# Kernel tuning notes

Measured on AMD Instinct MI355X. Metric: run time of the kernel, lower is better.

Reference implementation:

```python
import math
import jax, jax.numpy as jnp
import numpy as np

B, L, D, H, DK = 2, 2048, 1024, 16, 64
LATTICE = (4, 4)


def _build_neighbours(n_heads, shape):
    positions = [divmod(i, shape[1]) for i in range(n_heads)]
    idx = np.full((n_heads, 8), -1, dtype=np.int32)
    w = np.zeros((n_heads, 8), dtype=np.float32)
    for i, (r1, c1) in enumerate(positions):
        k = 0
        for dr in (-1, 0, 1):
            for dc in (-1, 0, 1):
                if dr == 0 and dc == 0:
                    continue
                if k >= 8:
                    break
                tgt = (r1 + dr, c1 + dc)
                for j, p in enumerate(positions):
                    if p == tgt:
                        idx[i, k] = j
                        w[i, k] = math.exp(-math.hypot(dr, dc))
                        k += 1
                        break
    return idx, w


def setup_inputs() -> dict:
    key = jax.random.key(0)
    ks = jax.random.split(key, 8)
    s = 1.0 / math.sqrt(D)  # typical linear init scale
    nb_idx, nb_w = _build_neighbours(H, LATTICE)
    return {
        "query": jax.random.normal(ks[0], (B, L, D), jnp.float32),
        "key": jax.random.normal(ks[1], (B, L, D), jnp.float32),
        "value": jax.random.normal(ks[2], (B, L, D), jnp.float32),
        "Wq": jax.random.normal(ks[3], (H, DK, D), jnp.float32) * s,
        "Wk": jax.random.normal(ks[4], (H, DK, D), jnp.float32) * s,
        "Wv": jax.random.normal(ks[5], (H, DK, D), jnp.float32) * s,
        "coupling_strength": jnp.full((H,), 0.1, jnp.float32),
        "out_w": jax.random.normal(ks[6], (D, D), jnp.float32) * s,
        "out_b": jnp.zeros((D,), jnp.float32),
        "neighbour_w": jnp.asarray(nb_w),
        "mask": jax.random.randint(ks[7], (B, L), 0, 2, jnp.int32),
        "neighbour_idx": jnp.asarray(nb_idx),
    }


def _phases(coupling_strength, neighbour_idx, neighbour_w):
    # Sequential Kuramoto update over heads (order matters: earlier heads'
    # updated phases are visible to later heads, as in the torch loop).
    freq = 1.0 + 0.1 * jnp.arange(H, dtype=jnp.float32)
    ph = jnp.zeros((H,), jnp.float32)
    two_pi = 2.0 * math.pi
    for i in range(H):  # H=16, structurally distinct sequential states
        nb = jnp.clip(neighbour_idx[i], 0, H - 1)  # invalid slots have w==0
        coupling = jnp.sum(neighbour_w[i] * jnp.sin(ph[nb] - ph[i]))
        new = jnp.mod(ph[i] + 0.01 * (freq[i] + coupling_strength[i] * coupling), two_pi)
        ph = ph.at[i].set(new)
    return ph


def reference(query, key, value, Wq, Wk, Wv, coupling_strength, out_w, out_b,
              neighbour_w, mask, neighbour_idx):
    ph = _phases(coupling_strength, neighbour_idx, neighbour_w)
    bias = 0.1 * jnp.cos(ph)  # [H] per-head scalar bias

    # Batched per-head projections: [B,L,D] x [H,DK,D] -> [B,H,L,DK]
    Q = jnp.einsum('bld,hkd->bhlk', query, Wq)
    K = jnp.einsum('bld,hkd->bhlk', key, Wk)
    V = jnp.einsum('bld,hkd->bhlk', value, Wv)

    scale = math.sqrt(float(DK))
    scores = jnp.einsum('bhqd,bhkd->bhqk', Q, K) / scale  # [B,H,L,L]
    scores = scores + bias[None, :, None, None]
    m = mask[:, None, None, :]  # [B,1,1,L], matches mask.unsqueeze(1).unsqueeze(1)
    scores = jnp.where(m == 0, jnp.float32(-10000.0), scores)
    attn = jax.nn.softmax(scores, axis=-1)
    out = jnp.einsum('bhqk,bhkd->bhqd', attn, V)  # [B,H,L,DK]
    out = out.transpose(0, 2, 1, 3).reshape(B, L, H * DK)  # concat heads
    return out @ out_w.T + out_b
```

## Files before the change

### kernel.cpp

```cpp
#include <hip/hip_runtime.h>
#include <hip/hip_fp16.h>


#define B_ 2
#define L_ 2048
#define D_ 1024
#define H_ 16
#define DK_ 64

#define QSCALE 0.1803368801111244f
#define MASKOFF -14427.0f

typedef _Float16 f16;
typedef _Float16 f16x2 __attribute__((ext_vector_type(2)));
typedef _Float16 f16x4 __attribute__((ext_vector_type(4)));
typedef _Float16 f16x8 __attribute__((ext_vector_type(8)));
typedef __fp16 hf16x2 __attribute__((ext_vector_type(2)));
typedef float f32x4 __attribute__((ext_vector_type(4)));

static __device__ __forceinline__ float fast_exp2(float x) {
    float r;
    asm("v_exp_f32 %0, %1" : "=v"(r) : "v"(x));
    return r;
}

static __device__ __forceinline__ f16x4 pack4(float a, float b, float c, float d) {
    hf16x2 lo = __builtin_amdgcn_cvt_pkrtz(a, b);
    hf16x2 hi = __builtin_amdgcn_cvt_pkrtz(c, d);
    f16x2 l2 = __builtin_bit_cast(f16x2, lo);
    f16x2 h2 = __builtin_bit_cast(f16x2, hi);
    f16x4 o; o[0] = l2[0]; o[1] = l2[1]; o[2] = h2[0]; o[3] = h2[1];
    return o;
}

__global__ __launch_bounds__(256) void qkv_proj_kernel(
    const float* __restrict__ query, const float* __restrict__ keyx,
    const float* __restrict__ value,
    const float* __restrict__ Wq, const float* __restrict__ Wk,
    const float* __restrict__ Wv,
    f16* __restrict__ Qh, f16* __restrict__ Kh, f16* __restrict__ VhT)
{
    const int z = blockIdx.z;
    const float* X = (z == 0) ? query : (z == 1) ? keyx : value;
    const float* W = (z == 0) ? Wq : (z == 1) ? Wk : Wv;
    f16* out = (z == 0) ? Qh : (z == 1) ? Kh : VhT;
    const float qs = (z == 0) ? QSCALE : 1.0f;

    const int m0 = blockIdx.x * 128;
    const int n0 = blockIdx.y * 128;
    const int tid = threadIdx.x;
    const int lane = tid & 63;
    const int w = tid >> 6;
    const int wr = (w >> 1) * 64, wc = (w & 1) * 64;

    __shared__ f16 As[2][128 * 40];
    __shared__ f16 Ws[2][128 * 40];

    f32x4 acc[4][4] = {};

    const int r = tid >> 3, c = (tid & 7) * 4;
    float4 ra[2][4], rb[2][4];

    auto issueK = [&](int kk) {
        #pragma unroll
        for (int s = 0; s < 2; ++s)
            #pragma unroll
            for (int p = 0; p < 4; ++p) {
                ra[s][p] = *(const float4*)&X[(size_t)(m0 + p * 32 + r) * D_ + kk + s * 32 + c];
                rb[s][p] = *(const float4*)&W[(size_t)(n0 + p * 32 + r) * D_ + kk + s * 32 + c];
            }
    };
    auto storeK = [&]() {
        #pragma unroll
        for (int s = 0; s < 2; ++s)
            #pragma unroll
            for (int p = 0; p < 4; ++p) {
                int row = p * 32 + r;
                f16x4 ha = { (f16)(ra[s][p].x * qs), (f16)(ra[s][p].y * qs),
                             (f16)(ra[s][p].z * qs), (f16)(ra[s][p].w * qs) };
                *(f16x4*)&As[s][row * 40 + c] = ha;
                f16x4 hb = { (f16)rb[s][p].x, (f16)rb[s][p].y,
                             (f16)rb[s][p].z, (f16)rb[s][p].w };
                *(f16x4*)&Ws[s][row * 40 + c] = hb;
            }
    };

    issueK(0);
    for (int t = 0; t < 16; ++t) {
        __syncthreads();
        storeK();
        if (t + 1 < 16) issueK((t + 1) * 64);
        __syncthreads();

        const int lg = (lane >> 4) * 8;
        #pragma unroll
        for (int s = 0; s < 2; ++s) {
            f16x8 af[4], bf[4];
            #pragma unroll
            for (int i = 0; i < 4; ++i) {
                af[i] = *(const f16x8*)&As[s][(wr + i * 16 + (lane & 15)) * 40 + lg];
                bf[i] = *(const f16x8*)&Ws[s][(wc + i * 16 + (lane & 15)) * 40 + lg];
            }
            #pragma unroll
            for (int i = 0; i < 4; ++i)
                #pragma unroll
                for (int j = 0; j < 4; ++j)
                    acc[i][j] = __builtin_amdgcn_mfma_f32_16x16x32_f16(af[i], bf[j], acc[i][j], 0, 0, 0);
        }
    }

    if (z == 2) {
        #pragma unroll
        for (int i = 0; i < 4; ++i) {
            int grow = m0 + wr + i * 16 + (lane >> 4) * 4;
            int b = grow >> 11, l = grow & (L_ - 1);
            #pragma unroll
            for (int j = 0; j < 4; ++j) {
                int gcol = n0 + wc + j * 16 + (lane & 15);
                int hh = gcol >> 6, k = gcol & 63;
                f16x4 o = { (f16)acc[i][j][0], (f16)acc[i][j][1],
                            (f16)acc[i][j][2], (f16)acc[i][j][3] };
                *(f16x4*)&out[((size_t)((b * H_ + hh) * DK_ + k)) * L_ + l] = o;
            }
        }
    } else {
        #pragma unroll
        for (int i = 0; i < 4; ++i) {
            int grow = m0 + wr + i * 16 + (lane >> 4) * 4;
            #pragma unroll
            for (int j = 0; j < 4; ++j) {
                int gcol = n0 + wc + j * 16 + (lane & 15);
                int hh = gcol >> 6, k = gcol & 63;
                #pragma unroll
                for (int rr = 0; rr < 4; ++rr) {
                    int row = grow + rr;
                    int b = row >> 11, l = row & (L_ - 1);
                    out[(((size_t)(b * H_ + hh)) * L_ + l) * DK_ + k] = (f16)acc[i][j][rr];
                }
            }
        }
    }
}

__global__ __launch_bounds__(256) void attn_kernel(
    const f16* __restrict__ Qh, const f16* __restrict__ Kh,
    const f16* __restrict__ VhT, const int* __restrict__ mask,
    f16* __restrict__ Oh)
{
    const int n = blockIdx.x;
    const int bh = ((n >> 7) << 3) + (n & 7);
    const int qb = (n >> 3) & 15;
    const int b = bh >> 4, h = bh & 15;
    const int q0 = qb * 128;
    const int tid = threadIdx.x;
    const int lane = tid & 63;
    const int w = tid >> 6;
    const int lq = lane & 15, g = lane >> 4;

    __shared__ f16 Ks[2][64 * 64];
    __shared__ f16 Vt[2][64 * 64];
    __shared__ f16 Plds[4][32 * 72];
    __shared__ float mofft[2][64];

    const size_t base = (size_t)bh * L_ * DK_;
    const int* maskp = mask + b * L_;

    f16x8 qf0[2], qf1[2];
    {
        const f16* qptr = Qh + base + (size_t)(q0 + w * 32 + lq) * DK_ + g * 8;
        qf0[0] = *(const f16x8*)(qptr);
        qf0[1] = *(const f16x8*)(qptr + 32);
        qptr += 16 * DK_;
        qf1[0] = *(const f16x8*)(qptr);
        qf1[1] = *(const f16x8*)(qptr + 32);
    }

    const int srow = tid >> 2;
    const int sslot = (tid & 3) * 2;
    const int ps0 = sslot ^ (srow & 7);
    const int ps1 = (sslot + 1) ^ (srow & 7);

    f32x4 acc0[4] = {}, acc1[4] = {};
    float mrun0 = -1e30f, lrun0 = 0.f;
    float mrun1 = -1e30f, lrun1 = 0.f;

    f16x8 kr0, kr1, vr0, vr1;

    auto issue = [&](int k0) {
        const f16* kp = Kh + base + (size_t)(k0 + srow) * DK_ + sslot * 8;
        kr0 = *(const f16x8*)kp;
        kr1 = *(const f16x8*)(kp + 8);
        const f16* vp = VhT + (size_t)(bh * DK_ + srow) * L_ + k0 + sslot * 8;
        vr0 = *(const f16x8*)vp;
        vr1 = *(const f16x8*)(vp + 8);
    };

    auto store_tile = [&](int buf, int k0) {
        *(f16x8*)&Ks[buf][srow * 64 + ps0 * 8] = kr0;
        *(f16x8*)&Ks[buf][srow * 64 + ps1 * 8] = kr1;
        *(f16x8*)&Vt[buf][srow * 64 + ps0 * 8] = vr0;
        *(f16x8*)&Vt[buf][srow * 64 + ps1 * 8] = vr1;
        if (tid < 16) {
            int4 mv = *(const int4*)&maskp[k0 + tid * 4];
            float4 f = { mv.x ? 0.f : MASKOFF, mv.y ? 0.f : MASKOFF,
                         mv.z ? 0.f : MASKOFF, mv.w ? 0.f : MASKOFF };
            *(float4*)&mofft[buf][tid * 4] = f;
        }
    };

    auto softmax_store = [&](float* sv, float& mrun, float& lrun,
                             f32x4* acc, int rowoff) {
        float a0 = fmaxf(sv[0], sv[1]),  a1 = fmaxf(sv[2], sv[3]);
        float a2 = fmaxf(sv[4], sv[5]),  a3 = fmaxf(sv[6], sv[7]);
        float a4 = fmaxf(sv[8], sv[9]),  a5 = fmaxf(sv[10], sv[11]);
        float a6 = fmaxf(sv[12], sv[13]), a7 = fmaxf(sv[14], sv[15]);
        float m = fmaxf(fmaxf(fmaxf(a0, a1), fmaxf(a2, a3)),
                        fmaxf(fmaxf(a4, a5), fmaxf(a6, a7)));
        m = fmaxf(m, __shfl_xor(m, 16, 64));
        m = fmaxf(m, __shfl_xor(m, 32, 64));
        if (__any(m > mrun)) {
            float mn = fmaxf(mrun, m);
            float scl = fast_exp2(mrun - mn);
            mrun = mn;
            lrun *= scl;
            #pragma unroll
            for (int f = 0; f < 4; ++f) acc[f] *= scl;
        }
        f16* pl = (f16*)Plds[w];
        float ls0 = 0.f, ls1 = 0.f;
        #pragma unroll
        for (int kt = 0; kt < 4; ++kt) {
            float p0 = fast_exp2(sv[kt * 4 + 0] - mrun);
            float p1 = fast_exp2(sv[kt * 4 + 1] - mrun);
            float p2 = fast_exp2(sv[kt * 4 + 2] - mrun);
            float p3 = fast_exp2(sv[kt * 4 + 3] - mrun);
            ls0 += p0 + p1;
            ls1 += p2 + p3;
            f16x4 pk = pack4(p0, p1, p2, p3);
            *(f16x4*)&pl[(rowoff + lq) * 72 + kt * 16 + g * 4] = pk;
        }
        lrun += ls0 + ls1;
    };

    auto compute = [&](int buf) {
        float sv0[16], sv1[16];
        __builtin_amdgcn_s_setprio(1);
        #pragma unroll
        for (int kt = 0; kt < 4; ++kt) {
            f32x4 cin = *(const f32x4*)&mofft[buf][kt * 16 + g * 4];
            int row = kt * 16 + lq;
            const f16* kb = &Ks[buf][row * 64];
            f16x8 a0 = *(const f16x8*)&kb[(g ^ (row & 7)) * 8];
            f16x8 a1 = *(const f16x8*)&kb[((g + 4) ^ (row & 7)) * 8];
            f32x4 s0 = __builtin_amdgcn_mfma_f32_16x16x32_f16(a0, qf0[0], cin, 0, 0, 0);
            s0 = __builtin_amdgcn_mfma_f32_16x16x32_f16(a1, qf0[1], s0, 0, 0, 0);
            f32x4 s1 = __builtin_amdgcn_mfma_f32_16x16x32_f16(a0, qf1[0], cin, 0, 0, 0);
            s1 = __builtin_amdgcn_mfma_f32_16x16x32_f16(a1, qf1[1], s1, 0, 0, 0);
            *(f32x4*)&sv0[kt * 4] = s0;
            *(f32x4*)&sv1[kt * 4] = s1;
        }
        __builtin_amdgcn_s_setprio(0);

        softmax_store(sv0, mrun0, lrun0, acc0, 0);
        softmax_store(sv1, mrun1, lrun1, acc1, 16);
        asm volatile("s_waitcnt lgkmcnt(0)" ::: "memory");
        __builtin_amdgcn_sched_barrier(0);

        f16* pl = (f16*)Plds[w];
        __builtin_amdgcn_s_setprio(1);
        #pragma unroll
        for (int kc = 0; kc < 2; ++kc) {
            f16x8 pb0 = *(const f16x8*)&pl[lq * 72 + kc * 32 + g * 8];
            f16x8 pb1 = *(const f16x8*)&pl[(16 + lq) * 72 + kc * 32 + g * 8];
            #pragma unroll
            for (int f = 0; f < 4; ++f) {
                int row = f * 16 + lq;
                f16x8 va = *(const f16x8*)&Vt[buf][row * 64 + ((kc * 4 + g) ^ (row & 7)) * 8];
                acc0[f] = __builtin_amdgcn_mfma_f32_16x16x32_f16(va, pb0, acc0[f], 0, 0, 0);
                acc1[f] = __builtin_amdgcn_mfma_f32_16x16x32_f16(va, pb1, acc1[f], 0, 0, 0);
            }
        }
        __builtin_amdgcn_s_setprio(0);
    };

    issue(0);
    store_tile(0, 0);
    issue(64);
    __syncthreads();

    #pragma unroll 2
    for (int t = 0; t < 32; ++t) {
        int buf = t & 1;
        if (t + 1 < 32) store_tile(buf ^ 1, (t + 1) * 64);
        if (t + 2 < 32) issue((t + 2) * 64);
        compute(buf);
        __syncthreads();
    }

    lrun0 += __shfl_xor(lrun0, 16, 64);
    lrun0 += __shfl_xor(lrun0, 32, 64);
    lrun1 += __shfl_xor(lrun1, 16, 64);
    lrun1 += __shfl_xor(lrun1, 32, 64);
    {
        float inv = 1.f / lrun0;
        int q = q0 + w * 32 + lq;
        #pragma unroll
        for (int f = 0; f < 4; ++f) {
            f16x4 o = { (f16)(acc0[f][0] * inv), (f16)(acc0[f][1] * inv),
                        (f16)(acc0[f][2] * inv), (f16)(acc0[f][3] * inv) };
            *(f16x4*)&Oh[((size_t)(b * L_ + q)) * D_ + h * 64 + f * 16 + g * 4] = o;
        }
    }
    {
        float inv = 1.f / lrun1;
        int q = q0 + w * 32 + 16 + lq;
        #pragma unroll
        for (int f = 0; f < 4; ++f) {
            f16x4 o = { (f16)(acc1[f][0] * inv), (f16)(acc1[f][1] * inv),
                        (f16)(acc1[f][2] * inv), (f16)(acc1[f][3] * inv) };
            *(f16x4*)&Oh[((size_t)(b * L_ + q)) * D_ + h * 64 + f * 16 + g * 4] = o;
        }
    }
}

__global__ __launch_bounds__(256) void out_proj_kernel(
    const f16* __restrict__ Oh, const float* __restrict__ outw,
    const float* __restrict__ outb, float* __restrict__ Y)
{
    const int m0 = blockIdx.x * 128;
    const int n0 = blockIdx.y * 128;
    const int tid = threadIdx.x;
    const int lane = tid & 63;
    const int w = tid >> 6;
    const int wr = (w >> 1) * 64, wc = (w & 1) * 64;

    __shared__ f16 As[2][128 * 40];
    __shared__ f16 Ws[2][128 * 40];

    f32x4 acc[4][4] = {};

    const int r = tid >> 3, c = (tid & 7) * 4;
    f16x4 ra[2][4];
    float4 rb[2][4];

    auto issueK = [&](int kk) {
        #pragma unroll
        for (int s = 0; s < 2; ++s)
            #pragma unroll
            for (int p = 0; p < 4; ++p) {
                ra[s][p] = *(const f16x4*)&Oh[(size_t)(m0 + p * 32 + r) * D_ + kk + s * 32 + c];
                rb[s][p] = *(const float4*)&outw[(size_t)(n0 + p * 32 + r) * D_ + kk + s * 32 + c];
            }
    };
    auto storeK = [&]() {
        #pragma unroll
        for (int s = 0; s < 2; ++s)
            #pragma unroll
            for (int p = 0; p < 4; ++p) {
                int row = p * 32 + r;
                *(f16x4*)&As[s][row * 40 + c] = ra[s][p];
                f16x4 hb = { (f16)rb[s][p].x, (f16)rb[s][p].y,
                             (f16)rb[s][p].z, (f16)rb[s][p].w };
                *(f16x4*)&Ws[s][row * 40 + c] = hb;
            }
    };

    issueK(0);
    for (int t = 0; t < 16; ++t) {
        __syncthreads();
        storeK();
        if (t + 1 < 16) issueK((t + 1) * 64);
        __syncthreads();

        const int lg = (lane >> 4) * 8;
        #pragma unroll
        for (int s = 0; s < 2; ++s) {
            f16x8 af[4], bf[4];
            #pragma unroll
            for (int i = 0; i < 4; ++i) {
                af[i] = *(const f16x8*)&As[s][(wr + i * 16 + (lane & 15)) * 40 + lg];
                bf[i] = *(const f16x8*)&Ws[s][(wc + i * 16 + (lane & 15)) * 40 + lg];
            }
            #pragma unroll
            for (int i = 0; i < 4; ++i)
                #pragma unroll
                for (int j = 0; j < 4; ++j)
                    acc[i][j] = __builtin_amdgcn_mfma_f32_16x16x32_f16(af[i], bf[j], acc[i][j], 0, 0, 0);
        }
    }

    #pragma unroll
    for (int i = 0; i < 4; ++i) {
        int grow = m0 + wr + i * 16 + (lane >> 4) * 4;
        #pragma unroll
        for (int j = 0; j < 4; ++j) {
            int gcol = n0 + wc + j * 16 + (lane & 15);
            float bias = outb[gcol];
            #pragma unroll
            for (int rr = 0; rr < 4; ++rr)
                Y[(size_t)(grow + rr) * D_ + gcol] = acc[i][j][rr] + bias;
        }
    }
}

extern "C" void kernel_launch(void* const* d_in, const int* in_sizes, int n_in,
                              void* d_out, int out_size, void* d_ws, size_t ws_size,
                              hipStream_t stream) {
    const float* query = (const float*)d_in[0];
    const float* key   = (const float*)d_in[1];
    const float* value = (const float*)d_in[2];
    const float* Wq    = (const float*)d_in[3];
    const float* Wk    = (const float*)d_in[4];
    const float* Wv    = (const float*)d_in[5];
    const float* outw  = (const float*)d_in[7];
    const float* outb  = (const float*)d_in[8];
    const int*   mask  = (const int*)d_in[10];
    float* Y = (float*)d_out;

    char* ws = (char*)d_ws;
    f16* Qh  = (f16*)(ws);
    f16* Kh  = (f16*)(ws + 8388608);
    f16* VhT = (f16*)(ws + 16777216);
    f16* Oh  = (f16*)(ws + 25165824);

    qkv_proj_kernel<<<dim3(32, 8, 3), 256, 0, stream>>>(query, key, value,
                                                        Wq, Wk, Wv, Qh, Kh, VhT);
    attn_kernel<<<dim3(512), 256, 0, stream>>>(Qh, Kh, VhT, mask, Oh);
    out_proj_kernel<<<dim3(32, 8), 256, 0, stream>>>(Oh, outw, outb, Y);
}
```

Before: 147.8 us.

## Split attention along the key dimension into two halves and merge

Each attention block now handles half of the key range, doubling the grid from 512 to 1024 blocks. Every block writes a partial normalized output plus its running max and sum, and a new merge kernel rescales and combines the two halves. The aim is better CU occupancy: 512 blocks on a 256-CU device gives poor wave balance. The cost is an extra kernel launch plus additional global traffic for the partial outputs and statistics, and a second f16 rounding of the output.

```diff
diff --git a/kernel.cpp b/kernel.cpp
--- a/kernel.cpp
+++ b/kernel.cpp
@@ -145,13 +145,16 @@
 __global__ __launch_bounds__(256) void attn_kernel(
     const f16* __restrict__ Qh, const f16* __restrict__ Kh,
     const f16* __restrict__ VhT, const int* __restrict__ mask,
-    f16* __restrict__ Oh)
+    f16* __restrict__ Ohalf, float* __restrict__ Mh, float* __restrict__ Lh)
 {
     const int n = blockIdx.x;
-    const int bh = ((n >> 7) << 3) + (n & 7);
-    const int qb = (n >> 3) & 15;
+    const int half = n >> 9;
+    const int n2 = n & 511;
+    const int bh = ((n2 >> 7) << 3) + (n2 & 7);
+    const int qb = (n2 >> 3) & 15;
     const int b = bh >> 4, h = bh & 15;
     const int q0 = qb * 128;
+    const int kbase = half * 1024;
     const int tid = threadIdx.x;
     const int lane = tid & 63;
     const int w = tid >> 6;
@@ -283,16 +286,16 @@
         __builtin_amdgcn_s_setprio(0);
     };
 
-    issue(0);
-    store_tile(0, 0);
-    issue(64);
+    issue(kbase);
+    store_tile(0, kbase);
+    issue(kbase + 64);
     __syncthreads();
 
     #pragma unroll 2
-    for (int t = 0; t < 32; ++t) {
+    for (int t = 0; t < 16; ++t) {
         int buf = t & 1;
-        if (t + 1 < 32) store_tile(buf ^ 1, (t + 1) * 64);
-        if (t + 2 < 32) issue((t + 2) * 64);
+        if (t + 1 < 16) store_tile(buf ^ 1, kbase + (t + 1) * 64);
+        if (t + 2 < 16) issue(kbase + (t + 2) * 64);
         compute(buf);
         __syncthreads();
     }
@@ -301,6 +304,8 @@
     lrun0 += __shfl_xor(lrun0, 32, 64);
     lrun1 += __shfl_xor(lrun1, 16, 64);
     lrun1 += __shfl_xor(lrun1, 32, 64);
+
+    f16* Ohp = Ohalf + (size_t)half * (B_ * L_ * D_);
     {
         float inv = 1.f / lrun0;
         int q = q0 + w * 32 + lq;
@@ -308,7 +313,7 @@
         for (int f = 0; f < 4; ++f) {
             f16x4 o = { (f16)(acc0[f][0] * inv), (f16)(acc0[f][1] * inv),
                         (f16)(acc0[f][2] * inv), (f16)(acc0[f][3] * inv) };
-            *(f16x4*)&Oh[((size_t)(b * L_ + q)) * D_ + h * 64 + f * 16 + g * 4] = o;
+            *(f16x4*)&Ohp[((size_t)(b * L_ + q)) * D_ + h * 64 + f * 16 + g * 4] = o;
         }
     }
     {
@@ -318,9 +323,44 @@
         for (int f = 0; f < 4; ++f) {
             f16x4 o = { (f16)(acc1[f][0] * inv), (f16)(acc1[f][1] * inv),
                         (f16)(acc1[f][2] * inv), (f16)(acc1[f][3] * inv) };
-            *(f16x4*)&Oh[((size_t)(b * L_ + q)) * D_ + h * 64 + f * 16 + g * 4] = o;
-        }
-    }
+            *(f16x4*)&Ohp[((size_t)(b * L_ + q)) * D_ + h * 64 + f * 16 + g * 4] = o;
+        }
+    }
+    if (g == 0) {
+        int q = q0 + w * 32 + lq;
+        int mlbase = half * (32 * L_) + bh * L_;
+        Mh[mlbase + q] = mrun0;
+        Lh[mlbase + q] = lrun0;
+        Mh[mlbase + q + 16] = mrun1;
+        Lh[mlbase + q + 16] = lrun1;
+    }
+}
+
+__global__ __launch_bounds__(256) void merge_kernel(
+    const f16* __restrict__ Ohalf, const float* __restrict__ Mh,
+    const float* __restrict__ Lh, f16* __restrict__ Oh)
+{
+    const int row = blockIdx.x;
+    const int b = row >> 11, l = row & (L_ - 1);
+    const int i = threadIdx.x * 4;
+    const int h = i >> 6;
+    const int idx = (b * H_ + h) * L_ + l;
+
+    float m1 = Mh[idx],             l1 = Lh[idx];
+    float m2 = Mh[32 * L_ + idx],   l2 = Lh[32 * L_ + idx];
+    float mx = fmaxf(m1, m2);
+    float w1 = l1 * fast_exp2(m1 - mx);
+    float w2 = l2 * fast_exp2(m2 - mx);
+    float inv = 1.f / (w1 + w2);
+    w1 *= inv; w2 *= inv;
+
+    f16x4 a = *(const f16x4*)&Ohalf[(size_t)row * D_ + i];
+    f16x4 c = *(const f16x4*)&Ohalf[(size_t)(B_ * L_) * D_ + (size_t)row * D_ + i];
+    f16x4 o;
+    #pragma unroll
+    for (int j = 0; j < 4; ++j)
+        o[j] = (f16)(w1 * (float)a[j] + w2 * (float)c[j]);
+    *(f16x4*)&Oh[(size_t)row * D_ + i] = o;
 }
 
 __global__ __launch_bounds__(256) void out_proj_kernel(
@@ -418,13 +458,17 @@
     float* Y = (float*)d_out;
 
     char* ws = (char*)d_ws;
-    f16* Qh  = (f16*)(ws);
-    f16* Kh  = (f16*)(ws + 8388608);
-    f16* VhT = (f16*)(ws + 16777216);
-    f16* Oh  = (f16*)(ws + 25165824);
+    f16* Qh    = (f16*)(ws);
+    f16* Kh    = (f16*)(ws + 8388608);
+    f16* VhT   = (f16*)(ws + 16777216);
+    f16* Oh    = (f16*)(ws + 25165824);
+    f16* Ohalf = (f16*)(ws + 33554432);
+    float* Mh  = (float*)(ws + 50331648);
+    float* Lh  = (float*)(ws + 50855936);
 
     qkv_proj_kernel<<<dim3(32, 8, 3), 256, 0, stream>>>(query, key, value,
                                                         Wq, Wk, Wv, Qh, Kh, VhT);
-    attn_kernel<<<dim3(512), 256, 0, stream>>>(Qh, Kh, VhT, mask, Oh);
+    attn_kernel<<<dim3(1024), 256, 0, stream>>>(Qh, Kh, VhT, mask, Ohalf, Mh, Lh);
+    merge_kernel<<<dim3(4096), 256, 0, stream>>>(Ohalf, Mh, Lh, Oh);
     out_proj_kernel<<<dim3(32, 8), 256, 0, stream>>>(Oh, outw, outb, Y);
 }
```

Measured after the change: 157.4 us. 6.5% more time.
